# Kernel tuning notes

Measured on AMD Instinct MI355X. Metric: run time of the kernel, lower is better.

Reference implementation:

```python
import jax, jax.numpy as jnp
import numpy as np

# DeepSeek-V2 router config
T = 8192          # tokens (batch*seq)
H = 5120          # hidden_size / gating_dim
E = 160           # n_routed_experts
N_GROUP = 8       # n_group
TOPK_GROUP = 3    # topk_group
TOP_K = 6         # num_experts_per_tok
SCALE = 16.0      # routed_scaling_factor (norm_topk_prob=False path)


def setup_inputs() -> dict:
    key = jax.random.key(0)
    k1, k2 = jax.random.split(key)
    hidden_states = jax.random.normal(k1, (T, H), dtype=jnp.float32)
    # kaiming_uniform init for the gating kernel
    bound = float(np.sqrt(6.0 / H))
    kernel = jax.random.uniform(k2, (E, H), dtype=jnp.float32, minval=-bound, maxval=bound)
    return {"hidden_states": hidden_states, "kernel": kernel}


def reference(hidden_states, kernel):
    # gating matmul in fp32: [T, H] @ [H, E] -> [T, E]
    logits = jnp.einsum("th,eh->te", hidden_states.astype(jnp.float32), kernel.astype(jnp.float32))
    scores = jax.nn.softmax(logits, axis=-1)  # [T, E]

    n_tok = scores.shape[0]
    # group-limited greedy: max score per group -> [T, N_GROUP]
    group_scores = scores.reshape(n_tok, N_GROUP, E // N_GROUP).max(axis=-1)
    top_group_idx = jax.lax.top_k(group_scores, TOPK_GROUP)[1]  # [T, TOPK_GROUP]

    # scatter 1s into selected groups
    row_idx = jnp.arange(n_tok)[:, None]
    group_mask = jnp.zeros_like(group_scores).at[row_idx, top_group_idx].set(1.0)  # [T, N_GROUP]

    # broadcast group mask over experts within each group -> [T, E]
    score_mask = jnp.repeat(group_mask[:, :, None], E // N_GROUP, axis=2).reshape(n_tok, -1)
    masked_scores = jnp.where(score_mask, scores, 0.0)

    topk_weight, _ = jax.lax.top_k(masked_scores, TOP_K)  # [T, TOP_K]
    # norm_topk_prob is False in DeepSeek-V2 -> scale by routed_scaling_factor
    return topk_weight * SCALE
```

## Files before the change

kernel.cpp:

```cpp
#include <hip/hip_runtime.h>
#include <math.h>

#define TT 8192
#define HH 5120
#define EE 160
#define NGRP 8
#define GSZ 20
#define TOPKG 3
#define TOPK 6
#define RSCALE 16.0f
#define SK 8
#define KS (HH / SK)
#define NSG (KS / 32)
#define BMG 128

typedef __attribute__((ext_vector_type(8))) short bf16x8;
typedef __attribute__((ext_vector_type(8))) _Float16 f16x8;
typedef __attribute__((ext_vector_type(4))) float f32x4;

#define BW_ELEMS ((size_t)160 * 10 * 64 * 8)
#define BWH_BYTES (BW_ELEMS * 2)

__device__ __forceinline__ ushort f2bf(float f) {
    uint32_t u = __float_as_uint(f);
    u += 0x7fff + ((u >> 16) & 1);
    return (ushort)(u >> 16);
}
__device__ __forceinline__ float bf2f(ushort h) {
    return __uint_as_float(((uint32_t)h) << 16);
}

__device__ __forceinline__ f16x8 cvt8(f32x4 x, f32x4 y) {
    f16x8 r;
    r[0] = (_Float16)x[0]; r[1] = (_Float16)x[1];
    r[2] = (_Float16)x[2]; r[3] = (_Float16)x[3];
    r[4] = (_Float16)y[0]; r[5] = (_Float16)y[1];
    r[6] = (_Float16)y[2]; r[7] = (_Float16)y[3];
    return r;
}

__global__ __launch_bounds__(256) void prep_b_f16(const float* __restrict__ B,
                                                  ushort* __restrict__ Bw) {
    int gid = blockIdx.x * 256 + threadIdx.x;
    int lane = gid & 63;
    int et   = (gid >> 6) % 10;
    int kt   = gid / 640;
    int e = et * 16 + (lane & 15);
    int c = kt * 32 + (lane >> 4) * 8;
    const float* src = B + (size_t)e * HH + c;
    f32x4 s0 = *(const f32x4*)src;
    f32x4 s1 = *(const f32x4*)(src + 4);
    union { f16x8 h; uint4 v; } u;
    u.h = cvt8(s0, s1);
    *reinterpret_cast<uint4*>(Bw + (size_t)gid * 8) = u.v;
}

__global__ __launch_bounds__(512, 4) void moe_gemm(const float* __restrict__ A,
                                                   const ushort* __restrict__ Bw,
                                                   float* __restrict__ P) {
    __shared__ char lds[2][10240];

    const int tid = threadIdx.x;
    const int w = tid >> 6, l = tid & 63;
    const int mb  = blockIdx.x & 63;
    const int ks  = blockIdx.x >> 6;
    const int bm0 = mb * BMG;
    const int kt0 = ks * NSG;

    const int row = l & 15, koct = l >> 4;

    const float* apA = A + (size_t)(bm0 + 16 * w + row) * HH + ks * KS + koct * 8;

    const char* BwB = (const char*)Bw;
    const int u0 = tid, u1 = tid + 512;

    f32x4 acc[10];
    #pragma unroll
    for (int et = 0; et < 10; et++) acc[et] = (f32x4){0.f, 0.f, 0.f, 0.f};

    {
        size_t tb = (size_t)kt0 * 10240;
        uint4 r0 = *(const uint4*)(BwB + tb + (size_t)u0 * 16);
        *(uint4*)(lds[0] + u0 * 16) = r0;
        if (tid < 128) {
            uint4 r1 = *(const uint4*)(BwB + tb + (size_t)u1 * 16);
            *(uint4*)(lds[0] + u1 * 16) = r1;
        }
    }
    f32x4 pa0 = *(const f32x4*)(apA), pa1 = *(const f32x4*)(apA + 4);
    __syncthreads();

    #pragma unroll 1
    for (int s = 0; s < NSG; ++s) {
        const int cur = s & 1;
        const bool more = (s + 1 < NSG);

        uint4 n0, n1;
        f32x4 na0 = pa0, na1 = pa1;
        if (more) {
            size_t tb = (size_t)(kt0 + s + 1) * 10240;
            n0 = *(const uint4*)(BwB + tb + (size_t)u0 * 16);
            if (tid < 128) n1 = *(const uint4*)(BwB + tb + (size_t)u1 * 16);
            const float* a = apA + (s + 1) * 32;
            na0 = *(const f32x4*)(a); na1 = *(const f32x4*)(a + 4);
        }

        f16x8 a16 = cvt8(pa0, pa1);
        const char* LB = lds[cur];
        #pragma unroll
        for (int et = 0; et < 10; ++et) {
            f16x8 bh = *(const f16x8*)(LB + et * 1024 + l * 16);
            acc[et] = __builtin_amdgcn_mfma_f32_16x16x32_f16(a16, bh, acc[et], 0, 0, 0);
        }

        if (more) {
            char* LN = lds[1 - cur];
            *(uint4*)(LN + u0 * 16) = n0;
            if (tid < 128) *(uint4*)(LN + u1 * 16) = n1;
        }
        pa0 = na0; pa1 = na1;
        __syncthreads();
    }

    const int rrow = koct * 4;
    #pragma unroll
    for (int et = 0; et < 10; et++)
        #pragma unroll
        for (int j = 0; j < 4; j++)
            P[((size_t)ks * TT + bm0 + 16 * w + rrow + j) * EE + et * 16 + row]
                = acc[et][j];
}

__global__ __launch_bounds__(512, 4) void moe_route(const float* __restrict__ P,
                                                    float* __restrict__ out) {
    const int w = threadIdx.x >> 6, l = threadIdx.x & 63;
    const int t = blockIdx.x * 8 + w;

    float s0 = 0.f, s1 = 0.f, s2 = 0.f;
    #pragma unroll
    for (int sl = 0; sl < SK; ++sl) {
        const float* b = P + ((size_t)sl * TT + t) * EE;
        s0 += b[l];
        s1 += b[64 + l];
        if (l < 32) s2 += b[128 + l];
    }
    if (l >= 32) s2 = -INFINITY;

    float m = fmaxf(s0, fmaxf(s1, s2));
    #pragma unroll
    for (int off = 32; off >= 1; off >>= 1) m = fmaxf(m, __shfl_xor(m, off, 64));
    float p0 = expf(s0 - m);
    float p1 = expf(s1 - m);
    float p2 = (l < 32) ? expf(s2 - m) : 0.f;
    float sum = p0 + p1 + p2;
    #pragma unroll
    for (int off = 32; off >= 1; off >>= 1) sum += __shfl_xor(sum, off, 64);
    float inv = 1.0f / sum;
    p0 *= inv; p1 *= inv; p2 *= inv;

    const int g0 = l / GSZ;
    const int g1 = (l + 64) / GSZ;
    const int g2 = (l + 128) / GSZ;

    float gmax[NGRP];
    #pragma unroll
    for (int g = 0; g < NGRP; g++) {
        float v = -1.f;
        if (g0 == g) v = p0;
        if (g1 == g) v = fmaxf(v, p1);
        if (l < 32 && g2 == g) v = fmaxf(v, p2);
        #pragma unroll
        for (int off = 32; off >= 1; off >>= 1) v = fmaxf(v, __shfl_xor(v, off, 64));
        gmax[g] = v;
    }

    int selmask = 0;
    #pragma unroll
    for (int s = 0; s < TOPKG; s++) {
        float best = -2.f; int bg = 0;
        #pragma unroll
        for (int g = 0; g < NGRP; g++)
            if (!((selmask >> g) & 1) && gmax[g] > best) { best = gmax[g]; bg = g; }
        selmask |= 1 << bg;
    }

    float m0 = ((selmask >> g0) & 1) ? p0 : 0.f;
    float m1 = ((selmask >> g1) & 1) ? p1 : 0.f;
    float m2 = (l < 32) ? (((selmask >> g2) & 1) ? p2 : 0.f) : -1.f;

    #pragma unroll
    for (int s = 0; s < TOPK; s++) {
        float v = fmaxf(m0, fmaxf(m1, m2));
        #pragma unroll
        for (int off = 32; off >= 1; off >>= 1) v = fmaxf(v, __shfl_xor(v, off, 64));
        int idx = 0x7fffffff;
        if (m0 == v) idx = l;
        if (m1 == v) idx = min(idx, l + 64);
        if (l < 32 && m2 == v) idx = min(idx, l + 128);
        #pragma unroll
        for (int off = 32; off >= 1; off >>= 1) idx = min(idx, __shfl_xor(idx, off, 64));
        if (idx == l)            m0 = -1.f;
        else if (idx == l + 64)  m1 = -1.f;
        else if (l < 32 && idx == l + 128) m2 = -1.f;
        if (l == 0) out[(size_t)t * TOPK + s] = v * RSCALE;
    }
}

#define BM 16
#define KW 640
#define NS (KW / 32)
#define PS (EE + 1)

__global__ __launch_bounds__(256) void prep_b_bf16(const float* __restrict__ B,
                                                   ushort* __restrict__ Bw) {
    int gid = blockIdx.x * 256 + threadIdx.x;
    int lane = gid & 63;
    int et   = (gid >> 6) % 10;
    int kt   = gid / 640;
    int e = et * 16 + (lane & 15);
    int c = kt * 32 + (lane >> 4) * 8;
    const float* src = B + (size_t)e * HH + c;
    uint4 vh, vl;
    uint32_t hw[8], lw[8];
    #pragma unroll
    for (int j = 0; j < 8; j++) {
        float f = src[j];
        ushort h = f2bf(f);
        float r = f - bf2f(h);
        hw[j] = h;
        lw[j] = f2bf(r);
    }
    vh.x = hw[0] | (hw[1] << 16); vh.y = hw[2] | (hw[3] << 16);
    vh.z = hw[4] | (hw[5] << 16); vh.w = hw[6] | (hw[7] << 16);
    vl.x = lw[0] | (lw[1] << 16); vl.y = lw[2] | (lw[3] << 16);
    vl.z = lw[4] | (lw[5] << 16); vl.w = lw[6] | (lw[7] << 16);
    *reinterpret_cast<uint4*>(Bw + (size_t)gid * 8) = vh;
    *reinterpret_cast<uint4*>(Bw + BW_ELEMS + (size_t)gid * 8) = vl;
}

__device__ __forceinline__ void split8(f32x4 x, f32x4 y, bf16x8& ah, bf16x8& al) {
    float fv[8] = {x[0], x[1], x[2], x[3], y[0], y[1], y[2], y[3]};
    union { uint32_t u[4]; bf16x8 v; } H, L;
    #pragma unroll
    for (int j = 0; j < 4; j++) {
        ushort h0 = f2bf(fv[2*j]), h1 = f2bf(fv[2*j+1]);
        float  r0 = fv[2*j]   - bf2f(h0);
        float  r1 = fv[2*j+1] - bf2f(h1);
        H.u[j] = (uint32_t)h0 | ((uint32_t)h1 << 16);
        L.u[j] = (uint32_t)f2bf(r0) | ((uint32_t)f2bf(r1) << 16);
    }
    ah = H.v; al = L.v;
}

__global__ __launch_bounds__(512, 4) void moe_mfma(const float* __restrict__ A,
                                                   const ushort* __restrict__ Bw,
                                                   float* __restrict__ out) {
    __shared__ float Sc[BM * PS];

    const int tid = threadIdx.x;
    const int w = tid >> 6, l = tid & 63;
    const int bm0 = blockIdx.x * BM;
    const int row  = l & 15;
    const int koct = l >> 4;

    f32x4 acc[10];
    #pragma unroll
    for (int et = 0; et < 10; et++) acc[et] = (f32x4){0.f, 0.f, 0.f, 0.f};

    const float* apw = A + (size_t)(bm0 + row) * HH + w * KW + koct * 8;

    #pragma unroll 1
    for (int s = 0; s < NS; ++s) {
        const f32x4* p = (const f32x4*)(apw + s * 32);
        bf16x8 ah, al;
        split8(p[0], p[1], ah, al);
        const ushort* bt = Bw + ((size_t)((w * NS + s) * 10) * 64 + (size_t)l) * 8;
        #pragma unroll
        for (int et = 0; et < 10; ++et) {
            bf16x8 bh = *(const bf16x8*)(bt + et * 512);
            bf16x8 bl = *(const bf16x8*)(bt + BW_ELEMS + et * 512);
            acc[et] = __builtin_amdgcn_mfma_f32_16x16x32_bf16(ah, bh, acc[et], 0, 0, 0);
            acc[et] = __builtin_amdgcn_mfma_f32_16x16x32_bf16(al, bh, acc[et], 0, 0, 0);
            acc[et] = __builtin_amdgcn_mfma_f32_16x16x32_bf16(ah, bl, acc[et], 0, 0, 0);
        }
    }

    for (int i = tid; i < BM * PS; i += 512) Sc[i] = 0.f;
    __syncthreads();
    const int rrow = koct * 4;
    #pragma unroll
    for (int et = 0; et < 10; et++)
        #pragma unroll
        for (int j = 0; j < 4; j++)
            atomicAdd(&Sc[(rrow + j) * PS + et * 16 + row], acc[et][j]);
    __syncthreads();

    for (int it = 0; it < 2; ++it) {
        const int r = w * 2 + it;
        float s0 = Sc[r * PS + l];
        float s1 = Sc[r * PS + 64 + l];
        float s2 = (l < 32) ? Sc[r * PS + 128 + l] : -INFINITY;

        float m = fmaxf(s0, fmaxf(s1, s2));
        #pragma unroll
        for (int off = 32; off >= 1; off >>= 1) m = fmaxf(m, __shfl_xor(m, off, 64));
        float p0 = expf(s0 - m);
        float p1 = expf(s1 - m);
        float p2 = (l < 32) ? expf(s2 - m) : 0.f;
        float sum = p0 + p1 + p2;
        #pragma unroll
        for (int off = 32; off >= 1; off >>= 1) sum += __shfl_xor(sum, off, 64);
        float inv = 1.0f / sum;
        p0 *= inv; p1 *= inv; p2 *= inv;

        const int g0 = l / GSZ;
        const int g1 = (l + 64) / GSZ;
        const int g2 = (l + 128) / GSZ;

        float gmax[NGRP];
        #pragma unroll
        for (int g = 0; g < NGRP; g++) {
            float v = -1.f;
            if (g0 == g) v = p0;
            if (g1 == g) v = fmaxf(v, p1);
            if (l < 32 && g2 == g) v = fmaxf(v, p2);
            #pragma unroll
            for (int off = 32; off >= 1; off >>= 1) v = fmaxf(v, __shfl_xor(v, off, 64));
            gmax[g] = v;
        }

        int selmask = 0;
        #pragma unroll
        for (int s = 0; s < TOPKG; s++) {
            float best = -2.f; int bg = 0;
            #pragma unroll
            for (int g = 0; g < NGRP; g++)
                if (!((selmask >> g) & 1) && gmax[g] > best) { best = gmax[g]; bg = g; }
            selmask |= 1 << bg;
        }

        float m0 = ((selmask >> g0) & 1) ? p0 : 0.f;
        float m1 = ((selmask >> g1) & 1) ? p1 : 0.f;
        float m2 = (l < 32) ? (((selmask >> g2) & 1) ? p2 : 0.f) : -1.f;

        #pragma unroll
        for (int s = 0; s < TOPK; s++) {
            float v = fmaxf(m0, fmaxf(m1, m2));
            #pragma unroll
            for (int off = 32; off >= 1; off >>= 1) v = fmaxf(v, __shfl_xor(v, off, 64));
            int idx = 0x7fffffff;
            if (m0 == v) idx = l;
            if (m1 == v) idx = min(idx, l + 64);
            if (l < 32 && m2 == v) idx = min(idx, l + 128);
            #pragma unroll
            for (int off = 32; off >= 1; off >>= 1) idx = min(idx, __shfl_xor(idx, off, 64));
            if (idx == l)            m0 = -1.f;
            else if (idx == l + 64)  m1 = -1.f;
            else if (l < 32 && idx == l + 128) m2 = -1.f;
            if (l == 0) out[(size_t)(bm0 + r) * TOPK + s] = v * RSCALE;
        }
    }
}

extern "C" void kernel_launch(void* const* d_in, const int* in_sizes, int n_in,
                              void* d_out, int out_size, void* d_ws, size_t ws_size,
                              hipStream_t stream) {
    const float* hs = (const float*)d_in[0];
    const float* kn = (const float*)d_in[1];
    float* o = (float*)d_out;

    const size_t pBytes = (size_t)SK * TT * EE * 4;
    if (ws_size >= BWH_BYTES + pBytes) {
        ushort* Bw = (ushort*)d_ws;
        float*  P  = (float*)((char*)d_ws + BWH_BYTES);
        hipLaunchKernelGGL(prep_b_f16, dim3(400),     dim3(256), 0, stream, kn, Bw);
        hipLaunchKernelGGL(moe_gemm,   dim3(64 * SK), dim3(512), 0, stream, hs, Bw, P);
        hipLaunchKernelGGL(moe_route,  dim3(TT / 8),  dim3(512), 0, stream, P, o);
    } else {
        ushort* Bw = (ushort*)d_ws;
        hipLaunchKernelGGL(prep_b_bf16, dim3(400),    dim3(256), 0, stream, kn, Bw);
        hipLaunchKernelGGL(moe_mfma,   dim3(TT / BM), dim3(512), 0, stream, hs, Bw, o);
    }
}
```

Before: 59.44 us.

## Reduce split-K partials with float atomics instead of a partial buffer

Replaces the split-K workspace of 8 partial logit slabs with a single logit buffer. Each GEMM block now adds its partial into that buffer with unsafeAtomicAdd, and the prep kernel zeroes the buffer first. The routing kernel reads one slab instead of summing eight. This cuts the global write and read traffic for partials, at the cost of atomic contention on the shared buffer, an extra zeroing pass, and a summation order that is no longer deterministic.

```diff
diff --git a/kernel.cpp b/kernel.cpp
--- a/kernel.cpp
+++ b/kernel.cpp
@@ -20,6 +20,7 @@
 
 #define BW_ELEMS ((size_t)160 * 10 * 64 * 8)
 #define BWH_BYTES (BW_ELEMS * 2)
+#define L_ELEMS  ((size_t)TT * EE)
 
 __device__ __forceinline__ ushort f2bf(float f) {
     uint32_t u = __float_as_uint(f);
@@ -40,8 +41,10 @@
 }
 
 __global__ __launch_bounds__(256) void prep_b_f16(const float* __restrict__ B,
-                                                  ushort* __restrict__ Bw) {
+                                                  ushort* __restrict__ Bw,
+                                                  float* __restrict__ L) {
     int gid = blockIdx.x * 256 + threadIdx.x;
+    for (size_t i = gid; i < L_ELEMS; i += 400 * 256) L[i] = 0.f;
     int lane = gid & 63;
     int et   = (gid >> 6) % 10;
     int kt   = gid / 640;
@@ -57,7 +60,7 @@
 
 __global__ __launch_bounds__(512, 4) void moe_gemm(const float* __restrict__ A,
                                                    const ushort* __restrict__ Bw,
-                                                   float* __restrict__ P) {
+                                                   float* __restrict__ L) {
     __shared__ char lds[2][10240];
 
     const int tid = threadIdx.x;
@@ -127,24 +130,19 @@
     for (int et = 0; et < 10; et++)
         #pragma unroll
         for (int j = 0; j < 4; j++)
-            P[((size_t)ks * TT + bm0 + 16 * w + rrow + j) * EE + et * 16 + row]
-                = acc[et][j];
-}
-
-__global__ __launch_bounds__(512, 4) void moe_route(const float* __restrict__ P,
+            unsafeAtomicAdd(&L[(size_t)(bm0 + 16 * w + rrow + j) * EE + et * 16 + row],
+                            acc[et][j]);
+}
+
+__global__ __launch_bounds__(512, 4) void moe_route(const float* __restrict__ L,
                                                     float* __restrict__ out) {
     const int w = threadIdx.x >> 6, l = threadIdx.x & 63;
     const int t = blockIdx.x * 8 + w;
 
-    float s0 = 0.f, s1 = 0.f, s2 = 0.f;
-    #pragma unroll
-    for (int sl = 0; sl < SK; ++sl) {
-        const float* b = P + ((size_t)sl * TT + t) * EE;
-        s0 += b[l];
-        s1 += b[64 + l];
-        if (l < 32) s2 += b[128 + l];
-    }
-    if (l >= 32) s2 = -INFINITY;
+    const float* b = L + (size_t)t * EE;
+    float s0 = b[l];
+    float s1 = b[64 + l];
+    float s2 = (l < 32) ? b[128 + l] : -INFINITY;
 
     float m = fmaxf(s0, fmaxf(s1, s2));
     #pragma unroll
@@ -369,13 +367,13 @@
     const float* kn = (const float*)d_in[1];
     float* o = (float*)d_out;
 
-    const size_t pBytes = (size_t)SK * TT * EE * 4;
-    if (ws_size >= BWH_BYTES + pBytes) {
+    const size_t lBytes = L_ELEMS * sizeof(float);
+    if (ws_size >= BWH_BYTES + lBytes) {
         ushort* Bw = (ushort*)d_ws;
-        float*  P  = (float*)((char*)d_ws + BWH_BYTES);
-        hipLaunchKernelGGL(prep_b_f16, dim3(400),     dim3(256), 0, stream, kn, Bw);
-        hipLaunchKernelGGL(moe_gemm,   dim3(64 * SK), dim3(512), 0, stream, hs, Bw, P);
-        hipLaunchKernelGGL(moe_route,  dim3(TT / 8),  dim3(512), 0, stream, P, o);
+        float*  L  = (float*)((char*)d_ws + BWH_BYTES);
+        hipLaunchKernelGGL(prep_b_f16, dim3(400),     dim3(256), 0, stream, kn, Bw, L);
+        hipLaunchKernelGGL(moe_gemm,   dim3(64 * SK), dim3(512), 0, stream, hs, Bw, L);
+        hipLaunchKernelGGL(moe_route,  dim3(TT / 8),  dim3(512), 0, stream, L, o);
     } else {
         ushort* Bw = (ushort*)d_ws;
         hipLaunchKernelGGL(prep_b_bf16, dim3(400),    dim3(256), 0, stream, kn, Bw);
```

Result: slower. 78.90 us (+32.7%).
